# Performance work log

Measured on AMD Instinct MI355X. Metric: run time of the kernel, lower is better.

The kernel has to match this reference:

```python
import jax, jax.numpy as jnp
import numpy as np

B, L, D = 16, 4096, 512
WORD_SIZE = 2048  # codebook_size // 4
WORD_LEN = 2


def setup_inputs() -> dict:
    key = jax.random.key(0)
    k1, k2, k3, k4, k5 = jax.random.split(key, 5)
    char_tokens = jax.random.randint(k1, (B, L), 0, 8192, dtype=jnp.int64 if jax.config.jax_enable_x64 else jnp.int32)
    char_embeddings = jax.random.normal(k2, (B, L, D), dtype=jnp.float32)
    # word_codebook initialized uniform(-1/word_size, 1/word_size) in the original
    word_codebook = jax.random.uniform(k3, (WORD_SIZE, D), dtype=jnp.float32,
                                       minval=-1.0 / WORD_SIZE, maxval=1.0 / WORD_SIZE)
    proj_w = jax.random.normal(k4, (D, D), dtype=jnp.float32) * (1.0 / np.sqrt(D))
    proj_b = jax.random.normal(k5, (D,), dtype=jnp.float32) * 0.01
    return {"char_tokens": char_tokens, "char_embeddings": char_embeddings,
            "word_codebook": word_codebook, "proj_w": proj_w, "proj_b": proj_b}


def reference(char_tokens, char_embeddings, word_codebook, proj_w, proj_b):
    Bv, Lv, Dv = char_embeddings.shape
    G = Lv // WORD_LEN  # number of 2-char groups per sequence
    # mean-pool each consecutive pair of characters -> [B, G, D]
    means = char_embeddings.reshape(Bv, G, WORD_LEN, Dv).mean(axis=2)
    # squared-euclidean nearest codebook entry (same argmin as cdist)
    # d2[b,g,k] = ||m||^2 - 2 m.W^T + ||W||^2 ; ||m||^2 constant over k -> drop
    dots = jnp.einsum('bgd,kd->bgk', means, word_codebook)            # [B,G,K]
    cb_sq = jnp.sum(word_codebook * word_codebook, axis=-1)           # [K]
    word_indices = jnp.argmin(cb_sq[None, None, :] - 2.0 * dots, axis=-1)  # [B,G]
    word_embeddings = word_codebook[word_indices]                     # [B,G,D]
    # alignment loss: mse(proj(word_emb), stop_grad(word_emb))
    projected = jnp.einsum('bgd,ed->bge', word_embeddings, proj_w) + proj_b
    target = jax.lax.stop_gradient(word_embeddings)
    alignment_loss = jnp.mean((projected - target) ** 2)
    return (word_indices, word_embeddings, alignment_loss)
```

## Files before the change

kernel.cpp:

```cpp
#include <hip/hip_runtime.h>


#define D_DIM    512
#define K_CODES  2048
#define N_ROWS   32768
#define EPS_GAP  1e-5f
#define LOSS_SCALE (1.0f / 16777216.0f)

typedef __attribute__((ext_vector_type(8))) short short8;
typedef __attribute__((ext_vector_type(4))) float f32x4;

__device__ __forceinline__ void split_bf16(float f, unsigned short& h, unsigned short& l) {
    unsigned u = __float_as_uint(f);
    h = (unsigned short)(u >> 16);
    float hr = __uint_as_float(u & 0xFFFF0000u);
    l = (unsigned short)(__float_as_uint(f - hr) >> 16);
}

__device__ __forceinline__ void dma16(const void* g, void* l) {
    __builtin_amdgcn_global_load_lds(
        (const __attribute__((address_space(1))) unsigned int*)g,
        (__attribute__((address_space(3))) unsigned int*)l, 16, 0, 0);
}

__device__ __forceinline__ void merge_cand(float s, int idx, float& v1, int& i1, float& v2, int& i2) {
    if (s < v1 || (s == v1 && idx < i1)) { v2 = v1; i2 = i1; v1 = s; i1 = idx; }
    else if (s < v2 || (s == v2 && idx < i2)) { v2 = s; i2 = idx; }
}

__global__ __launch_bounds__(256, 1)
void cra_pack(const float* __restrict__ cb,
              unsigned short* __restrict__ wsBh,
              unsigned short* __restrict__ wsBl,
              float* __restrict__ cb_sq)
{
    __shared__ float cbs[32 * D_DIM];
    const int tid = threadIdx.x;
    const int c0  = blockIdx.x * 32;

    {
        const float4* src = (const float4*)(cb + (size_t)c0 * D_DIM);
        float4* dst = (float4*)cbs;
        #pragma unroll
        for (int k = 0; k < 16; ++k) dst[tid + k * 256] = src[tid + k * 256];
    }
    __syncthreads();

    if (tid < 32) {
        const float* r = cbs + tid * D_DIM;
        float s = 0.f;
        for (int d = 0; d < D_DIM; ++d) s = fmaf(r[d], r[d], s);
        cb_sq[c0 + tid] = s;
    }

    const int row = tid >> 3;
    const int k   = c0 + row;
    const int colb = k >> 8;
    const int pr   = k & 255;
    const int d0   = (tid & 7) * 64;
    #pragma unroll
    for (int g = 0; g < 8; ++g) {
        const int d = d0 + g * 8;
        const int cchunk = d >> 5;
        const int s = d & 31;
        short8 h8, l8;
        #pragma unroll
        for (int e = 0; e < 8; ++e) {
            unsigned short hh, ll;
            split_bf16(cbs[row * D_DIM + d + e], hh, ll);
            h8[e] = (short)hh; l8[e] = (short)ll;
        }
        const size_t off = (size_t)colb * 131072 + cchunk * 8192 + pr * 32 + s;
        *(short8*)(wsBh + off) = h8;
        *(short8*)(wsBl + off) = l8;
    }
}

__global__ __launch_bounds__(256, 1)
void cra_proj(const float* __restrict__ cb,
              const float* __restrict__ W,
              const float* __restrict__ pb,
              float* __restrict__ Sk)
{
    __shared__ float cbs[32 * D_DIM];
    __shared__ float red[4 * 32];
    const int tid = threadIdx.x;
    const int cblock = blockIdx.x >> 2;
    const int eb     = blockIdx.x & 3;
    const int c0 = cblock * 32;

    {
        const float4* src = (const float4*)(cb + (size_t)c0 * D_DIM);
        float4* dst = (float4*)cbs;
        #pragma unroll
        for (int k = 0; k < 16; ++k) dst[tid + k * 256] = src[tid + k * 256];
    }
    __syncthreads();

    const int e  = eb * 128 + (tid >> 1);
    const int dh = (tid & 1) * 256;
    float acc[32];
    #pragma unroll
    for (int c = 0; c < 32; ++c) acc[c] = 0.f;
    const float4* wrow = (const float4*)(W + (size_t)e * D_DIM + dh);
    for (int dq = 0; dq < 64; ++dq) {
        const float4 wv = wrow[dq];
        #pragma unroll
        for (int c = 0; c < 32; ++c) {
            const float4 cv = *(const float4*)&cbs[c * D_DIM + dh + dq * 4];
            acc[c] += cv.x * wv.x + cv.y * wv.y + cv.z * wv.z + cv.w * wv.w;
        }
    }
    const float bias = pb[e];
    const int w = tid >> 6;
    #pragma unroll
    for (int c = 0; c < 32; ++c) {
        const float full = acc[c] + __shfl_xor(acc[c], 1);
        const float diff = full + bias - cbs[c * D_DIM + e];
        float v = (tid & 1) ? 0.f : diff * diff;
        #pragma unroll
        for (int off = 32; off > 0; off >>= 1) v += __shfl_down(v, off, 64);
        if ((tid & 63) == 0) red[w * 32 + c] = v;
    }
    __syncthreads();
    if (tid < 32)
        atomicAdd(&Sk[c0 + tid],
                  red[tid] + red[32 + tid] + red[64 + tid] + red[96 + tid]);
}

__global__ __launch_bounds__(512, 4)
void cra_gemm(const float* __restrict__ ce,
              const unsigned short* __restrict__ wsBh,
              const unsigned short* __restrict__ wsBl,
              const float* __restrict__ cb_sq,
              float4* __restrict__ wsRed)
{
    __shared__ short sMem[24576];
    short* sAh = sMem;
    short* sAl = sMem + 4096;
    short* sBh = sMem + 8192;
    short* sBl = sMem + 16384;

    const int tid  = threadIdx.x;
    const int bid  = blockIdx.x;
    const int xcd  = bid & 7;
    const int slot = bid >> 3;
    const int mb   = xcd * 32 + (slot >> 3);
    const int colb = slot & 7;
    const int rowBase = mb * 128;
    const int colBase = colb * 256;

    const int lane = tid & 63;
    const int w    = tid >> 6;
    const int wr   = (w & 1) * 64;
    const int cw   = w >> 1;
    const int wc   = cw * 64;
    const int cid  = lane & 15;
    const int quad = lane >> 4;

    f32x4 acc[4][4];
    #pragma unroll
    for (int i = 0; i < 4; ++i)
        #pragma unroll
        for (int j = 0; j < 4; ++j) acc[i][j] = (f32x4)(0.f);

    const int srow = tid >> 2;
    const int sA   = (tid & 3) * 8;
    const float* a0p = ce + (size_t)(2 * (rowBase + srow)) * D_DIM + sA;
    const float* a1p = a0p + D_DIM;

    const char* gBh = (const char*)wsBh + ((size_t)colb << 18);
    const char* gBl = (const char*)wsBl + ((size_t)colb << 18);
    char* lBh = (char*)sBh + w * 2048;
    char* lBl = (char*)sBl + w * 2048;
    const int gwoff = w * 2048 + lane * 16;

    float4 pa[4];
    pa[0] = *(const float4*)(a0p);     pa[1] = *(const float4*)(a0p + 4);
    pa[2] = *(const float4*)(a1p);     pa[3] = *(const float4*)(a1p + 4);

    #pragma unroll 1
    for (int c = 0; c < 16; ++c) {
        {
            const char* gh = gBh + c * 16384 + gwoff;
            const char* gl = gBl + c * 16384 + gwoff;
            dma16(gh,        lBh);
            dma16(gh + 1024, lBh + 1024);
            dma16(gl,        lBl);
            dma16(gl + 1024, lBl + 1024);
        }
        {
            float m[8];
            m[0] = 0.5f * (pa[0].x + pa[2].x); m[1] = 0.5f * (pa[0].y + pa[2].y);
            m[2] = 0.5f * (pa[0].z + pa[2].z); m[3] = 0.5f * (pa[0].w + pa[2].w);
            m[4] = 0.5f * (pa[1].x + pa[3].x); m[5] = 0.5f * (pa[1].y + pa[3].y);
            m[6] = 0.5f * (pa[1].z + pa[3].z); m[7] = 0.5f * (pa[1].w + pa[3].w);
            short8 h8, l8;
            #pragma unroll
            for (int e = 0; e < 8; ++e) {
                unsigned short hh, ll;
                split_bf16(m[e], hh, ll);
                h8[e] = (short)hh; l8[e] = (short)ll;
            }
            *(short8*)&sAh[srow * 32 + sA] = h8;
            *(short8*)&sAl[srow * 32 + sA] = l8;
        }
        __syncthreads();

        if (c < 15) {
            const int k0 = (c + 1) * 32;
            pa[0] = *(const float4*)(a0p + k0);     pa[1] = *(const float4*)(a0p + k0 + 4);
            pa[2] = *(const float4*)(a1p + k0);     pa[3] = *(const float4*)(a1p + k0 + 4);
        }

        short8 aF[4], bF[4];
        #pragma unroll
        for (int mi = 0; mi < 4; ++mi) aF[mi] = *(const short8*)&sAh[(wr + mi * 16 + cid) * 32 + quad * 8];
        #pragma unroll
        for (int ni = 0; ni < 4; ++ni) bF[ni] = *(const short8*)&sBh[(wc + ni * 16 + cid) * 32 + quad * 8];
        #pragma unroll
        for (int mi = 0; mi < 4; ++mi)
            #pragma unroll
            for (int ni = 0; ni < 4; ++ni)
                acc[mi][ni] = __builtin_amdgcn_mfma_f32_16x16x32_bf16(aF[mi], bF[ni], acc[mi][ni], 0, 0, 0);
        #pragma unroll
        for (int mi = 0; mi < 4; ++mi) aF[mi] = *(const short8*)&sAl[(wr + mi * 16 + cid) * 32 + quad * 8];
        #pragma unroll
        for (int mi = 0; mi < 4; ++mi)
            #pragma unroll
            for (int ni = 0; ni < 4; ++ni)
                acc[mi][ni] = __builtin_amdgcn_mfma_f32_16x16x32_bf16(aF[mi], bF[ni], acc[mi][ni], 0, 0, 0);
        #pragma unroll
        for (int mi = 0; mi < 4; ++mi) aF[mi] = *(const short8*)&sAh[(wr + mi * 16 + cid) * 32 + quad * 8];
        #pragma unroll
        for (int ni = 0; ni < 4; ++ni) bF[ni] = *(const short8*)&sBl[(wc + ni * 16 + cid) * 32 + quad * 8];
        #pragma unroll
        for (int mi = 0; mi < 4; ++mi)
            #pragma unroll
            for (int ni = 0; ni < 4; ++ni)
                acc[mi][ni] = __builtin_amdgcn_mfma_f32_16x16x32_bf16(aF[mi], bF[ni], acc[mi][ni], 0, 0, 0);
        __syncthreads();
    }

    float cq[4];
    #pragma unroll
    for (int ni = 0; ni < 4; ++ni) cq[ni] = cb_sq[colBase + wc + ni * 16 + cid];

    float4* sRed = (float4*)sMem;
    #pragma unroll
    for (int mi = 0; mi < 4; ++mi) {
        #pragma unroll
        for (int reg = 0; reg < 4; ++reg) {
            float v1 = 3.4e38f, v2 = 3.4e38f;
            int   i1 = 0x7FFFFFFF, i2 = 0x7FFFFFFF;
            #pragma unroll
            for (int ni = 0; ni < 4; ++ni) {
                const float s = fmaf(-2.0f, acc[mi][ni][reg], cq[ni]);
                merge_cand(s, colBase + wc + ni * 16 + cid, v1, i1, v2, i2);
            }
            #pragma unroll
            for (int d = 1; d <= 2; d <<= 1) {
                float ov1 = __shfl_xor(v1, d); int oi1 = __shfl_xor(i1, d);
                float ov2 = __shfl_xor(v2, d); int oi2 = __shfl_xor(i2, d);
                merge_cand(ov1, oi1, v1, i1, v2, i2);
                merge_cand(ov2, oi2, v1, i1, v2, i2);
            }
            if ((cid & 3) == 0) {
                const int row = wr + mi * 16 + quad * 4 + reg;
                sRed[(row * 4 + cw) * 4 + (cid >> 2)] =
                    make_float4(v1, __int_as_float(i1), v2, __int_as_float(i2));
            }
        }
    }
    __syncthreads();
    if (tid < 128) {
        float v1 = 3.4e38f, v2 = 3.4e38f;
        int   i1 = 0x7FFFFFFF, i2 = 0x7FFFFFFF;
        #pragma unroll
        for (int e = 0; e < 16; ++e) {
            const float4 t = sRed[tid * 16 + e];
            merge_cand(t.x, __float_as_int(t.y), v1, i1, v2, i2);
            merge_cand(t.z, __float_as_int(t.w), v1, i1, v2, i2);
        }
        wsRed[(size_t)(rowBase + tid) * 8 + colb] =
            make_float4(v1, __int_as_float(i1), v2, __int_as_float(i2));
    }
}

__global__ __launch_bounds__(256, 1)
void cra_merge(const float4* __restrict__ wsRed,
               const float* __restrict__ Sk,
               float* __restrict__ out_idx,
               float* __restrict__ out_loss,
               int* __restrict__ counter,
               int* __restrict__ flagRow,
               int2* __restrict__ flagI)
{
    __shared__ float sl[256];
    const int tid = threadIdx.x;
    const int r = blockIdx.x * 256 + tid;
    float v1 = 3.4e38f, v2 = 3.4e38f;
    int   i1 = 0x7FFFFFFF, i2 = 0x7FFFFFFF;
    #pragma unroll
    for (int cbk = 0; cbk < 8; ++cbk) {
        const float4 t = wsRed[(size_t)r * 8 + cbk];
        merge_cand(t.x, __float_as_int(t.y), v1, i1, v2, i2);
        merge_cand(t.z, __float_as_int(t.w), v1, i1, v2, i2);
    }
    out_idx[r] = (float)i1;
    if (v2 - v1 < EPS_GAP) {
        const int slot = atomicAdd(counter, 1);
        flagRow[slot] = r;
        flagI[slot] = make_int2(i1, i2);
    }
    sl[tid] = Sk[i1];
    __syncthreads();
    for (int s = 128; s > 0; s >>= 1) { if (tid < s) sl[tid] += sl[tid + s]; __syncthreads(); }
    if (tid == 0) atomicAdd(out_loss, sl[0] * LOSS_SCALE);
}

__global__ __launch_bounds__(256, 1)
void cra_gather(const float* __restrict__ out_idx,
                const float4* __restrict__ cb4,
                float4* __restrict__ out4)
{
    __shared__ int sidx[128];
    const int tid = threadIdx.x;
    const int rb = blockIdx.x * 128;
    if (tid < 128) sidx[tid] = (int)out_idx[rb + tid];
    __syncthreads();
    for (int j = tid; j < 128 * 128; j += 256) {
        const int row = j >> 7, q = j & 127;
        out4[(size_t)(rb + row) * 128 + q] = cb4[(size_t)sidx[row] * 128 + q];
    }
}

__global__ __launch_bounds__(256, 1)
void cra_recheck(const float* __restrict__ ce,
                 const float* __restrict__ cb,
                 const float* __restrict__ cb_sq,
                 const float* __restrict__ Sk,
                 const int* __restrict__ counter,
                 const int* __restrict__ flagRow,
                 const int2* __restrict__ flagI,
                 float* __restrict__ out_idx,
                 float4* __restrict__ out4,
                 float* __restrict__ out_loss,
                 const float4* __restrict__ cb4)
{
    __shared__ float rp[8];
    __shared__ int swin;
    const int tid = threadIdx.x;
    const int n = counter[0];
    for (int f = blockIdx.x; f < n; f += 64) {
        const int row = flagRow[f];
        const int2 ii = flagI[f];
        const int d0 = tid * 2;
        const float2 x0 = *(const float2*)(ce + (size_t)(2 * row) * D_DIM + d0);
        const float2 x1 = *(const float2*)(ce + (size_t)(2 * row) * D_DIM + D_DIM + d0);
        const float m0 = 0.5f * (x0.x + x1.x), m1 = 0.5f * (x0.y + x1.y);
        const float* c1 = cb + (size_t)ii.x * D_DIM + d0;
        const float* c2 = cb + (size_t)ii.y * D_DIM + d0;
        float p1 = fmaf(m0, c1[0], m1 * c1[1]);
        float p2 = fmaf(m0, c2[0], m1 * c2[1]);
        #pragma unroll
        for (int off = 32; off > 0; off >>= 1) {
            p1 += __shfl_down(p1, off, 64);
            p2 += __shfl_down(p2, off, 64);
        }
        if ((tid & 63) == 0) { rp[(tid >> 6) * 2] = p1; rp[(tid >> 6) * 2 + 1] = p2; }
        __syncthreads();
        if (tid == 0) {
            const float dot1 = rp[0] + rp[2] + rp[4] + rp[6];
            const float dot2 = rp[1] + rp[3] + rp[5] + rp[7];
            const float s1 = cb_sq[ii.x] - 2.f * dot1;
            const float s2 = cb_sq[ii.y] - 2.f * dot2;
            const int win = (s2 < s1 || (s2 == s1 && ii.y < ii.x)) ? ii.y : ii.x;
            swin = win;
            if (win != ii.x) {
                out_idx[row] = (float)win;
                atomicAdd(out_loss, (Sk[win] - Sk[ii.x]) * LOSS_SCALE);
            }
        }
        __syncthreads();
        if (swin != ii.x) {
            for (int q = tid; q < 128; q += 256)
                out4[(size_t)row * 128 + q] = cb4[(size_t)swin * 128 + q];
        }
        __syncthreads();
    }
}

extern "C" void kernel_launch(void* const* d_in, const int* in_sizes, int n_in,
                              void* d_out, int out_size, void* d_ws, size_t ws_size,
                              hipStream_t stream)
{
    const float* ce = (const float*)d_in[1];
    const float* cb = (const float*)d_in[2];
    const float* W  = (const float*)d_in[3];
    const float* pb = (const float*)d_in[4];

    char* ws = (char*)d_ws;
    unsigned short* wsBh = (unsigned short*)ws;
    unsigned short* wsBl = (unsigned short*)(ws + 2097152);
    float* cb_sq   = (float*)(ws + 4194304);
    float* Sk      = (float*)(ws + 4194304 + 8192);
    int*   flagRow = (int*)(ws + 4194304 + 16384);
    int2*  flagI   = (int2*)(ws + 4194304 + 16384 + 131072);
    int*   counter = (int*)(ws + 4194304 + 16384 + 131072 + 262144);

    float* out_idx  = (float*)d_out;
    float* out_emb  = out_idx + N_ROWS;
    float* out_loss = out_emb + (size_t)N_ROWS * D_DIM;
    float4* wsRed   = (float4*)out_emb;

    hipMemsetAsync(Sk, 0, K_CODES * sizeof(float), stream);
    hipMemsetAsync(counter, 0, sizeof(int), stream);
    hipMemsetAsync(out_loss, 0, sizeof(float), stream);

    cra_pack<<<64, 256, 0, stream>>>(cb, wsBh, wsBl, cb_sq);
    cra_proj<<<256, 256, 0, stream>>>(cb, W, pb, Sk);
    cra_gemm<<<2048, 512, 0, stream>>>(ce, wsBh, wsBl, cb_sq, wsRed);
    cra_merge<<<128, 256, 0, stream>>>(wsRed, Sk, out_idx, out_loss, counter, flagRow, flagI);
    cra_gather<<<256, 256, 0, stream>>>(out_idx, (const float4*)cb, (float4*)out_emb);
    cra_recheck<<<64, 256, 0, stream>>>(ce, cb, cb_sq, Sk, counter, flagRow, flagI,
                                        out_idx, (float4*)out_emb, out_loss, (const float4*)cb);
}
```

Before: 950.8 us.

## Pre-pack pooled A into bf16 hi/lo tiles and restructure split-bf16 GEMM

Result: faster. 867.4 us (-8.8%).

```diff
diff --git a/kernel.cpp b/kernel.cpp
--- a/kernel.cpp
+++ b/kernel.cpp
@@ -29,14 +29,68 @@
 }
 
 __global__ __launch_bounds__(256, 1)
-void cra_pack(const float* __restrict__ cb,
-              unsigned short* __restrict__ wsBh,
-              unsigned short* __restrict__ wsBl,
-              float* __restrict__ cb_sq)
+void cra_pack_a(const float* __restrict__ ce,
+                unsigned short* __restrict__ Ap)
+{
+    const int tid = threadIdx.x;
+    const int mb  = blockIdx.x;
+    const int rq  = tid >> 5;
+    const int dq  = tid & 31;
+    const int dbase = dq * 16;
+    const int ach = dq >> 1;
+    const int k0  = (dq & 1) * 16;
+
+    #pragma unroll 2
+    for (int p = 0; p < 16; ++p) {
+        const int r  = p * 8 + rq;
+        const int gr = mb * 128 + r;
+        const float* a0 = ce + (size_t)(2 * gr) * D_DIM + dbase;
+        const float* a1 = a0 + D_DIM;
+        float4 x0[4], x1[4];
+        #pragma unroll
+        for (int q = 0; q < 4; ++q) {
+            x0[q] = *(const float4*)(a0 + q * 4);
+            x1[q] = *(const float4*)(a1 + q * 4);
+        }
+        short8 h8[2], l8[2];
+        #pragma unroll
+        for (int q = 0; q < 4; ++q) {
+            const float m[4] = {0.5f * (x0[q].x + x1[q].x), 0.5f * (x0[q].y + x1[q].y),
+                                0.5f * (x0[q].z + x1[q].z), 0.5f * (x0[q].w + x1[q].w)};
+            #pragma unroll
+            for (int e = 0; e < 4; ++e) {
+                unsigned short hh, ll;
+                split_bf16(m[e], hh, ll);
+                h8[q >> 1][(q & 1) * 4 + e] = (short)hh;
+                l8[q >> 1][(q & 1) * 4 + e] = (short)ll;
+            }
+        }
+        const size_t hb = ((size_t)(mb * 32 + ach) * 128 + r) * 32 + k0;
+        const size_t lb = ((size_t)(mb * 32 + 16 + ach) * 128 + r) * 32 + k0;
+        *(short8*)(Ap + hb)     = h8[0];
+        *(short8*)(Ap + hb + 8) = h8[1];
+        *(short8*)(Ap + lb)     = l8[0];
+        *(short8*)(Ap + lb + 8) = l8[1];
+    }
+}
+
+__global__ __launch_bounds__(256, 1)
+void cra_pack_b(const float* __restrict__ cb,
+                unsigned short* __restrict__ Bp,
+                float* __restrict__ cb_sq,
+                float* __restrict__ Sk,
+                int* __restrict__ counter,
+                float* __restrict__ loss_out)
 {
     __shared__ float cbs[32 * D_DIM];
     const int tid = threadIdx.x;
     const int c0  = blockIdx.x * 32;
+
+    if (blockIdx.x == 0) {
+        #pragma unroll
+        for (int j = 0; j < 8; ++j) Sk[tid + j * 256] = 0.0f;
+        if (tid == 0) { counter[0] = 0; loss_out[0] = 0.0f; }
+    }
 
     {
         const float4* src = (const float4*)(cb + (size_t)c0 * D_DIM);
@@ -53,16 +107,16 @@
         cb_sq[c0 + tid] = s;
     }
 
-    const int row = tid >> 3;
-    const int k   = c0 + row;
-    const int colb = k >> 8;
-    const int pr   = k & 255;
-    const int d0   = (tid & 7) * 64;
+    const int row  = tid >> 3;
+    const int k    = c0 + row;
+    const int colb = k >> 7;
+    const int pr   = k & 127;
+    const int dspan = (tid & 7) * 64;
     #pragma unroll
     for (int g = 0; g < 8; ++g) {
-        const int d = d0 + g * 8;
-        const int cchunk = d >> 5;
-        const int s = d & 31;
+        const int d   = dspan + g * 8;
+        const int bch = d >> 5;
+        const int k0  = d & 31;
         short8 h8, l8;
         #pragma unroll
         for (int e = 0; e < 8; ++e) {
@@ -70,9 +124,8 @@
             split_bf16(cbs[row * D_DIM + d + e], hh, ll);
             h8[e] = (short)hh; l8[e] = (short)ll;
         }
-        const size_t off = (size_t)colb * 131072 + cchunk * 8192 + pr * 32 + s;
-        *(short8*)(wsBh + off) = h8;
-        *(short8*)(wsBl + off) = l8;
+        *(short8*)(Bp + ((size_t)(colb * 32 + bch) * 128 + pr) * 32 + k0)      = h8;
+        *(short8*)(Bp + ((size_t)(colb * 32 + 16 + bch) * 128 + pr) * 32 + k0) = l8;
     }
 }
 
@@ -128,33 +181,30 @@
                   red[tid] + red[32 + tid] + red[64 + tid] + red[96 + tid]);
 }
 
-__global__ __launch_bounds__(512, 4)
-void cra_gemm(const float* __restrict__ ce,
-              const unsigned short* __restrict__ wsBh,
-              const unsigned short* __restrict__ wsBl,
+__global__ __launch_bounds__(256, 3)
+void cra_gemm(const unsigned short* __restrict__ Ap,
+              const unsigned short* __restrict__ Bp,
               const float* __restrict__ cb_sq,
               float4* __restrict__ wsRed)
 {
-    __shared__ short sMem[24576];
-    short* sAh = sMem;
-    short* sAl = sMem + 4096;
-    short* sBh = sMem + 8192;
-    short* sBl = sMem + 16384;
+    __shared__ short sMem[8192];
+    short* sA = sMem;
+    short* sB = sMem + 4096;
 
     const int tid  = threadIdx.x;
     const int bid  = blockIdx.x;
     const int xcd  = bid & 7;
     const int slot = bid >> 3;
-    const int mb   = xcd * 32 + (slot >> 3);
-    const int colb = slot & 7;
+    const int mb   = xcd * 32 + (slot >> 4);
+    const int colb = slot & 15;
     const int rowBase = mb * 128;
-    const int colBase = colb * 256;
+    const int colBase = colb * 128;
 
     const int lane = tid & 63;
     const int w    = tid >> 6;
     const int wr   = (w & 1) * 64;
-    const int cw   = w >> 1;
-    const int wc   = cw * 64;
+    const int wcH  = w >> 1;
+    const int wc   = wcH * 64;
     const int cid  = lane & 15;
     const int quad = lane >> 4;
 
@@ -164,76 +214,28 @@
         #pragma unroll
         for (int j = 0; j < 4; ++j) acc[i][j] = (f32x4)(0.f);
 
-    const int srow = tid >> 2;
-    const int sA   = (tid & 3) * 8;
-    const float* a0p = ce + (size_t)(2 * (rowBase + srow)) * D_DIM + sA;
-    const float* a1p = a0p + D_DIM;
-
-    const char* gBh = (const char*)wsBh + ((size_t)colb << 18);
-    const char* gBl = (const char*)wsBl + ((size_t)colb << 18);
-    char* lBh = (char*)sBh + w * 2048;
-    char* lBl = (char*)sBl + w * 2048;
-    const int gwoff = w * 2048 + lane * 16;
-
-    float4 pa[4];
-    pa[0] = *(const float4*)(a0p);     pa[1] = *(const float4*)(a0p + 4);
-    pa[2] = *(const float4*)(a1p);     pa[3] = *(const float4*)(a1p + 4);
+    const char* Ag = (const char*)Ap + ((size_t)mb   * 32) * 8192 + w * 2048 + lane * 16;
+    const char* Bg = (const char*)Bp + ((size_t)colb * 32) * 8192 + w * 2048 + lane * 16;
+    char* lA = (char*)sA + w * 2048;
+    char* lB = (char*)sB + w * 2048;
 
     #pragma unroll 1
-    for (int c = 0; c < 16; ++c) {
-        {
-            const char* gh = gBh + c * 16384 + gwoff;
-            const char* gl = gBl + c * 16384 + gwoff;
-            dma16(gh,        lBh);
-            dma16(gh + 1024, lBh + 1024);
-            dma16(gl,        lBl);
-            dma16(gl + 1024, lBl + 1024);
-        }
-        {
-            float m[8];
-            m[0] = 0.5f * (pa[0].x + pa[2].x); m[1] = 0.5f * (pa[0].y + pa[2].y);
-            m[2] = 0.5f * (pa[0].z + pa[2].z); m[3] = 0.5f * (pa[0].w + pa[2].w);
-            m[4] = 0.5f * (pa[1].x + pa[3].x); m[5] = 0.5f * (pa[1].y + pa[3].y);
-            m[6] = 0.5f * (pa[1].z + pa[3].z); m[7] = 0.5f * (pa[1].w + pa[3].w);
-            short8 h8, l8;
-            #pragma unroll
-            for (int e = 0; e < 8; ++e) {
-                unsigned short hh, ll;
-                split_bf16(m[e], hh, ll);
-                h8[e] = (short)hh; l8[e] = (short)ll;
-            }
-            *(short8*)&sAh[srow * 32 + sA] = h8;
-            *(short8*)&sAl[srow * 32 + sA] = l8;
-        }
+    for (int g = 0; g < 48; ++g) {
+        const int ach = g & 31;
+        const int bch = (g & 15) | ((g & 32) >> 1);
+        const char* ag = Ag + ach * 8192;
+        const char* bg = Bg + bch * 8192;
+        dma16(ag,        lA);
+        dma16(ag + 1024, lA + 1024);
+        dma16(bg,        lB);
+        dma16(bg + 1024, lB + 1024);
         __syncthreads();
 
-        if (c < 15) {
-            const int k0 = (c + 1) * 32;
-            pa[0] = *(const float4*)(a0p + k0);     pa[1] = *(const float4*)(a0p + k0 + 4);
-            pa[2] = *(const float4*)(a1p + k0);     pa[3] = *(const float4*)(a1p + k0 + 4);
-        }
-
         short8 aF[4], bF[4];
         #pragma unroll
-        for (int mi = 0; mi < 4; ++mi) aF[mi] = *(const short8*)&sAh[(wr + mi * 16 + cid) * 32 + quad * 8];
-        #pragma unroll
-        for (int ni = 0; ni < 4; ++ni) bF[ni] = *(const short8*)&sBh[(wc + ni * 16 + cid) * 32 + quad * 8];
-        #pragma unroll
-        for (int mi = 0; mi < 4; ++mi)
-            #pragma unroll
-            for (int ni = 0; ni < 4; ++ni)
-                acc[mi][ni] = __builtin_amdgcn_mfma_f32_16x16x32_bf16(aF[mi], bF[ni], acc[mi][ni], 0, 0, 0);
-        #pragma unroll
-        for (int mi = 0; mi < 4; ++mi) aF[mi] = *(const short8*)&sAl[(wr + mi * 16 + cid) * 32 + quad * 8];
-        #pragma unroll
-        for (int mi = 0; mi < 4; ++mi)
-            #pragma unroll
-            for (int ni = 0; ni < 4; ++ni)
-                acc[mi][ni] = __builtin_amdgcn_mfma_f32_16x16x32_bf16(aF[mi], bF[ni], acc[mi][ni], 0, 0, 0);
-        #pragma unroll
-        for (int mi = 0; mi < 4; ++mi) aF[mi] = *(const short8*)&sAh[(wr + mi * 16 + cid) * 32 + quad * 8];
-        #pragma unroll
-        for (int ni = 0; ni < 4; ++ni) bF[ni] = *(const short8*)&sBl[(wc + ni * 16 + cid) * 32 + quad * 8];
+        for (int mi = 0; mi < 4; ++mi) aF[mi] = *(const short8*)&sA[(wr + mi * 16 + cid) * 32 + quad * 8];
+        #pragma unroll
+        for (int ni = 0; ni < 4; ++ni) bF[ni] = *(const short8*)&sB[(wc + ni * 16 + cid) * 32 + quad * 8];
         #pragma unroll
         for (int mi = 0; mi < 4; ++mi)
             #pragma unroll
@@ -267,7 +269,7 @@
             }
             if ((cid & 3) == 0) {
                 const int row = wr + mi * 16 + quad * 4 + reg;
-                sRed[(row * 4 + cw) * 4 + (cid >> 2)] =
+                sRed[(row * 2 + wcH) * 4 + (cid >> 2)] =
                     make_float4(v1, __int_as_float(i1), v2, __int_as_float(i2));
             }
         }
@@ -277,12 +279,12 @@
         float v1 = 3.4e38f, v2 = 3.4e38f;
         int   i1 = 0x7FFFFFFF, i2 = 0x7FFFFFFF;
         #pragma unroll
-        for (int e = 0; e < 16; ++e) {
-            const float4 t = sRed[tid * 16 + e];
+        for (int e = 0; e < 8; ++e) {
+            const float4 t = sRed[tid * 8 + e];
             merge_cand(t.x, __float_as_int(t.y), v1, i1, v2, i2);
             merge_cand(t.z, __float_as_int(t.w), v1, i1, v2, i2);
         }
-        wsRed[(size_t)(rowBase + tid) * 8 + colb] =
+        wsRed[(size_t)(rowBase + tid) * 16 + colb] =
             make_float4(v1, __int_as_float(i1), v2, __int_as_float(i2));
     }
 }
@@ -301,9 +303,9 @@
     const int r = blockIdx.x * 256 + tid;
     float v1 = 3.4e38f, v2 = 3.4e38f;
     int   i1 = 0x7FFFFFFF, i2 = 0x7FFFFFFF;
-    #pragma unroll
-    for (int cbk = 0; cbk < 8; ++cbk) {
-        const float4 t = wsRed[(size_t)r * 8 + cbk];
+    #pragma unroll 4
+    for (int cbk = 0; cbk < 16; ++cbk) {
+        const float4 t = wsRed[(size_t)r * 16 + cbk];
         merge_cand(t.x, __float_as_int(t.y), v1, i1, v2, i2);
         merge_cand(t.z, __float_as_int(t.w), v1, i1, v2, i2);
     }
@@ -401,26 +403,23 @@
     const float* pb = (const float*)d_in[4];
 
     char* ws = (char*)d_ws;
-    unsigned short* wsBh = (unsigned short*)ws;
-    unsigned short* wsBl = (unsigned short*)(ws + 2097152);
-    float* cb_sq   = (float*)(ws + 4194304);
-    float* Sk      = (float*)(ws + 4194304 + 8192);
-    int*   flagRow = (int*)(ws + 4194304 + 16384);
-    int2*  flagI   = (int2*)(ws + 4194304 + 16384 + 131072);
-    int*   counter = (int*)(ws + 4194304 + 16384 + 131072 + 262144);
+    unsigned short* Bp = (unsigned short*)ws;
+    float4* wsRed  = (float4*)(ws + 4194304);
+    float* cb_sq   = (float*)(ws + 12582912);
+    float* Sk      = (float*)(ws + 12582912 + 8192);
+    int*   flagRow = (int*)(ws + 12582912 + 16384);
+    int2*  flagI   = (int2*)(ws + 12582912 + 16384 + 131072);
+    int*   counter = (int*)(ws + 12582912 + 16384 + 131072 + 262144);
 
     float* out_idx  = (float*)d_out;
     float* out_emb  = out_idx + N_ROWS;
     float* out_loss = out_emb + (size_t)N_ROWS * D_DIM;
-    float4* wsRed   = (float4*)out_emb;
-
-    hipMemsetAsync(Sk, 0, K_CODES * sizeof(float), stream);
-    hipMemsetAsync(counter, 0, sizeof(int), stream);
-    hipMemsetAsync(out_loss, 0, sizeof(float), stream);
-
-    cra_pack<<<64, 256, 0, stream>>>(cb, wsBh, wsBl, cb_sq);
+    unsigned short* Ap = (unsigned short*)out_emb;
+
+    cra_pack_a<<<256, 256, 0, stream>>>(ce, Ap);
+    cra_pack_b<<<64, 256, 0, stream>>>(cb, Bp, cb_sq, Sk, counter, out_loss);
     cra_proj<<<256, 256, 0, stream>>>(cb, W, pb, Sk);
-    cra_gemm<<<2048, 512, 0, stream>>>(ce, wsBh, wsBl, cb_sq, wsRed);
+    cra_gemm<<<4096, 256, 0, stream>>>(Ap, Bp, cb_sq, wsRed);
     cra_merge<<<128, 256, 0, stream>>>(wsRed, Sk, out_idx, out_loss, counter, flagRow, flagI);
     cra_gather<<<256, 256, 0, stream>>>(out_idx, (const float4*)cb, (float4*)out_emb);
     cra_recheck<<<64, 256, 0, stream>>>(ce, cb, cb_sq, Sk, counter, flagRow, flagI,
```
